# Optimization experiments

Hardware: AMD Instinct MI355X
Metric: run time of the kernel (lower is better)

Reference implementation:

```python
import jax, jax.numpy as jnp
import numpy as np

H = 1024      # hidden_dim
NH = 16       # num_heads
HD = H // NH  # head_dim
FF = 4 * H
EPS = 1e-5

def _ln(x, g, b):
    m = jnp.mean(x, axis=-1, keepdims=True)
    v = jnp.var(x, axis=-1, keepdims=True)
    return (x - m) * jax.lax.rsqrt(v + EPS) * g + b

def setup_inputs() -> dict:
    key = jax.random.key(0)
    ks = jax.random.split(key, 12)
    s = 1.0 / np.sqrt(H)
    inp = {
        'x': jax.random.normal(ks[0], (2, 2048, H), dtype=jnp.float32),
        'Wq': jax.random.normal(ks[1], (H, H), dtype=jnp.float32) * s,
        'bq': jnp.zeros((H,), dtype=jnp.float32),
        'Wk': jax.random.normal(ks[2], (H, H), dtype=jnp.float32) * s,
        'bk': jnp.zeros((H,), dtype=jnp.float32),
        'Wv': jax.random.normal(ks[3], (H, H), dtype=jnp.float32) * s,
        'bv': jnp.zeros((H,), dtype=jnp.float32),
        'Wo': jax.random.normal(ks[4], (H, H), dtype=jnp.float32) * s,
        'bo': jnp.zeros((H,), dtype=jnp.float32),
        'g1': jnp.ones((H,), dtype=jnp.float32),
        'b1': jnp.zeros((H,), dtype=jnp.float32),
        'W1': jax.random.normal(ks[5], (H, FF), dtype=jnp.float32) * s,
        'bf1': jnp.zeros((FF,), dtype=jnp.float32),
        'W2': jax.random.normal(ks[6], (FF, H), dtype=jnp.float32) * (1.0 / np.sqrt(FF)),
        'bf2': jnp.zeros((H,), dtype=jnp.float32),
        'g2': jnp.ones((H,), dtype=jnp.float32),
        'b2': jnp.zeros((H,), dtype=jnp.float32),
    }
    return inp

def reference(x, Wq, bq, Wk, bk, Wv, bv, Wo, bo, g1, b1, W1, bf1, W2, bf2, g2, b2):
    B, S, _ = x.shape
    residual = x
    xn = _ln(x, g1, b1)
    # [B,S,H] -> [B,NH,S,HD]
    def split_heads(t):
        return t.reshape(B, S, NH, HD).transpose(0, 2, 1, 3)
    q = split_heads(xn @ Wq + bq)
    k = split_heads(xn @ Wk + bk)
    v = split_heads(xn @ Wv + bv)
    scores = jnp.einsum('bhqd,bhkd->bhqk', q, k) / np.sqrt(HD).astype(np.float32)
    attn = jax.nn.softmax(scores, axis=-1)
    ctx = jnp.einsum('bhqk,bhkd->bhqd', attn, v)
    ctx = ctx.transpose(0, 2, 1, 3).reshape(B, S, H)
    out = ctx @ Wo + bo + residual
    residual = out
    on = _ln(out, g2, b2)
    out = jax.nn.relu(on @ W1 + bf1) @ W2 + bf2 + residual
    return out
```

## Files before the change

### kernel.cpp

```cpp
#include <hip/hip_runtime.h>
#include <hip/hip_bf16.h>

constexpr int HDIM = 1024;
constexpr int NHEAD = 16;
constexpr int FFDIM = 4096;
constexpr int SEQLEN = 2048;
constexpr int NTOK = 4096;

typedef __bf16 bf16x8 __attribute__((ext_vector_type(8)));
typedef float f32x4 __attribute__((ext_vector_type(4)));
typedef short s16x4 __attribute__((ext_vector_type(4)));

union U16x8 {
    s16x4 h[2];
    bf16x8 v;
    int4 raw;
    unsigned u[4];
    short s[8];
};

__device__ __forceinline__ short f2bf(float f) {
    union { float f; unsigned u; } c;
    c.f = f;
    return (short)((c.u + 0x8000u) >> 16);
}
__device__ __forceinline__ float bf2f(short s) {
    union { unsigned u; float f; } c;
    c.u = ((unsigned)(unsigned short)s) << 16;
    return c.f;
}

__device__ __forceinline__ unsigned cvtpk(float a, float b) {
    __hip_bfloat162 h = __float22bfloat162_rn(float2{a, b});
    return *reinterpret_cast<unsigned*>(&h);
}

__device__ __forceinline__ float exp2_raw(float x) {
    float r;
    asm("v_exp_f32 %0, %1" : "=v"(r) : "v"(x));
    return r;
}

template <int N>
__device__ __forceinline__ void wait_vmcnt() {
    if constexpr (N == 0) asm volatile("s_waitcnt vmcnt(0)" ::: "memory");
    else if constexpr (N == 8) asm volatile("s_waitcnt vmcnt(8)" ::: "memory");
    else if constexpr (N == 16) asm volatile("s_waitcnt vmcnt(16)" ::: "memory");
    else static_assert(N == 0 || N == 8 || N == 16, "unsupported vmcnt");
}
__device__ __forceinline__ void barrier_fence() {
    __builtin_amdgcn_s_barrier();
    asm volatile("" ::: "memory");
}

__device__ __forceinline__ void gload16(const void* gsrc, void* lds) {
    __builtin_amdgcn_global_load_lds(
        (const __attribute__((address_space(1))) unsigned int*)gsrc,
        (__attribute__((address_space(3))) unsigned int*)lds, 16, 0, 0);
}


constexpr float QSCALE = 0.18033688011112042f;

__device__ __forceinline__ void ln_store(float (&vv)[16], const float* g,
                                         const float* b, short* orow, int lane,
                                         float mean, float rstd) {
#pragma unroll
    for (int i = 0; i < 4; ++i) {
        const int c = i * 256 + lane * 4;
        float4 gv = *(const float4*)&g[c];
        float4 bv = *(const float4*)&b[c];
        union { s16x4 h4; uint2 u2; } pk;
        pk.u2.x = cvtpk((vv[i * 4 + 0] - mean) * rstd * gv.x + bv.x,
                        (vv[i * 4 + 1] - mean) * rstd * gv.y + bv.y);
        pk.u2.y = cvtpk((vv[i * 4 + 2] - mean) * rstd * gv.z + bv.z,
                        (vv[i * 4 + 3] - mean) * rstd * gv.w + bv.w);
        const int kk = c & 31;
        const int dst = (c & ~31) + ((kk & 15) >> 2) * 8 + (kk >> 4) * 4;
        *(s16x4*)&orow[dst] = pk.h4;
    }
}

__device__ __forceinline__ void ln_row(const float* __restrict__ xr,
                                       const float* __restrict__ g,
                                       const float* __restrict__ b,
                                       short* __restrict__ orow, int lane) {
    float vv[16];
    float s = 0.0f, ss = 0.0f;
#pragma unroll
    for (int i = 0; i < 4; ++i) {
        float4 v = *(const float4*)&xr[i * 256 + lane * 4];
        vv[i * 4] = v.x; vv[i * 4 + 1] = v.y; vv[i * 4 + 2] = v.z; vv[i * 4 + 3] = v.w;
        s += v.x + v.y + v.z + v.w;
        ss += v.x * v.x + v.y * v.y + v.z * v.z + v.w * v.w;
    }
#pragma unroll
    for (int o = 32; o > 0; o >>= 1) {
        s += __shfl_xor(s, o);
        ss += __shfl_xor(ss, o);
    }
    const float mean = s * (1.0f / HDIM);
    const float rstd = rsqrtf(ss * (1.0f / HDIM) - mean * mean + 1e-5f);
    ln_store(vv, g, b, orow, lane, mean, rstd);
}

__device__ __forceinline__ void ln_row_b(const short* __restrict__ xr,
                                         const float* __restrict__ g,
                                         const float* __restrict__ b,
                                         short* __restrict__ orow, int lane) {
    float vv[16];
    float s = 0.0f, ss = 0.0f;
#pragma unroll
    for (int i = 0; i < 4; ++i) {
        s16x4 h = *(const s16x4*)&xr[i * 256 + lane * 4];
#pragma unroll
        for (int j = 0; j < 4; ++j) {
            const float f = bf2f(h[j]);
            vv[i * 4 + j] = f;
            s += f;
            ss += f * f;
        }
    }
#pragma unroll
    for (int o = 32; o > 0; o >>= 1) {
        s += __shfl_xor(s, o);
        ss += __shfl_xor(ss, o);
    }
    const float mean = s * (1.0f / HDIM);
    const float rstd = rsqrtf(ss * (1.0f / HDIM) - mean * mean + 1e-5f);
    ln_store(vv, g, b, orow, lane, mean, rstd);
}

__global__ __launch_bounds__(256)
void wconv_all(const float* __restrict__ Wq, const float* __restrict__ Wk,
               const float* __restrict__ Wv, const float* __restrict__ Wo,
               const float* __restrict__ W1, const float* __restrict__ W2,
               short* __restrict__ qkvT, short* __restrict__ WoT,
               short* __restrict__ W1T, short* __restrict__ W2T,
               const float* __restrict__ x, const float* __restrict__ g1,
               const float* __restrict__ b1, short* __restrict__ xn) {
    int i = blockIdx.x;
    if (i >= 6144) {
        const int wave = threadIdx.x >> 6, lane = threadIdx.x & 63;
        const int row = (i - 6144) * 4 + wave;
        ln_row(x + (size_t)row * HDIM, g1, b1, xn + (size_t)row * HDIM, lane);
        return;
    }
    const float* W;
    short* WT;
    int K, N, bx, by;
    if (i < 2048) {
        const int w = i >> 9;
        i &= 511;
        K = HDIM; N = HDIM; bx = i & 3; by = i >> 2;
        W = w == 0 ? Wq : w == 1 ? Wk : w == 2 ? Wv : Wo;
        WT = w == 3 ? WoT : qkvT + (size_t)w * HDIM * HDIM;
    } else if (i < 4096) {
        i -= 2048;
        K = HDIM; N = FFDIM; bx = i & 15; by = i >> 4;
        W = W1; WT = W1T;
    } else {
        i -= 4096;
        K = FFDIM; N = HDIM; bx = i & 3; by = i >> 2;
        W = W2; WT = W2T;
    }
    const int n = bx * 256 + threadIdx.x;
    const int g = by >> 2, fc = by & 3;
    const int k0 = g * 32 + fc * 4;
    float a[4], c[4];
#pragma unroll
    for (int j = 0; j < 4; ++j) a[j] = W[(size_t)(k0 + j) * N + n];
#pragma unroll
    for (int j = 0; j < 4; ++j) c[j] = W[(size_t)(k0 + 16 + j) * N + n];
    U16x8 u;
    u.u[0] = cvtpk(a[0], a[1]);
    u.u[1] = cvtpk(a[2], a[3]);
    u.u[2] = cvtpk(c[0], c[1]);
    u.u[3] = cvtpk(c[2], c[3]);
    *(int4*)(WT + (size_t)n * K + by * 8) = u.raw;
}

__global__ __launch_bounds__(256)
void ln_bf16b(const short* __restrict__ x, const float* __restrict__ g,
              const float* __restrict__ b, short* __restrict__ out) {
    const int wave = threadIdx.x >> 6, lane = threadIdx.x & 63;
    const int row = blockIdx.x * 4 + wave;
    ln_row_b(x + (size_t)row * HDIM, g, b, out + (size_t)row * HDIM, lane);
}

template <int BM, int BN, int MODE, int PIPE>
__global__ __launch_bounds__(256, (PIPE == 3) ? 1 : (PIPE ? 2 : (((BM + BN) == 256) ? 3 : 4)))
void gemm_bf16(const short* __restrict__ A, const short* __restrict__ BT,
               const float* __restrict__ bias, const void* __restrict__ resid,
               void* __restrict__ outp, int M, int N, int K,
               const float* __restrict__ bias2, const float* __restrict__ bias3,
               void* __restrict__ out3) {
    constexpr int MI = BM / 32, NJ = BN / 32;
    constexpr int NSEG = (BM + BN) / 16;
    constexpr int PW = NSEG / 4;
    constexpr int BUFS = (BM + BN) * 32;
    constexpr int NBUF = (PIPE == 3) ? 8 : (PIPE == 2) ? 4 : 2;
    static_assert(PIPE < 2 || (BM + BN) == 256, "PIPE>=2 tuned for PW=4");
    __shared__ short LdsF[NBUF * BUFS];
    const int tid = threadIdx.x;
    const int lane = tid & 63, wave = tid >> 6;
    const int wm = wave >> 1, wn = wave & 1;
    const int l15 = lane & 15, lg = lane >> 4;
    const int lsw = lg ^ ((l15 >> 1) & 3);
    const int m0 = blockIdx.x * BM, n0 = blockIdx.y * BN;
    const int nk = K >> 5;
    const int sr = lane >> 2;
    const int sc8 = (((lane & 3) ^ ((sr >> 1) & 3))) * 8;

    auto stage = [&](int buf, int kt) {
#pragma unroll
        for (int p = 0; p < PW; ++p) {
            const int s = wave + p * 4;
            const short* src = (s < BM / 16)
                ? A + (size_t)(m0 + s * 16 + sr) * K + kt * 32 + sc8
                : BT + (size_t)(n0 + (s - BM / 16) * 16 + sr) * K + kt * 32 + sc8;
            const int off = __builtin_amdgcn_readfirstlane(buf * BUFS * 2 + s * 1024);
            gload16(src, (char*)LdsF + off);
        }
    };
    auto compute = [&](int buf, f32x4 (&acc)[MI][NJ]) {
        bf16x8 af[MI], bfr[NJ];
#pragma unroll
        for (int i = 0; i < MI; ++i)
            af[i] = *(const bf16x8*)&LdsF[buf * BUFS +
                                          (wm * (BM / 2) + i * 16 + l15) * 32 + lsw * 8];
#pragma unroll
        for (int j = 0; j < NJ; ++j)
            bfr[j] = *(const bf16x8*)&LdsF[buf * BUFS +
                                           (BM + wn * (BN / 2) + j * 16 + l15) * 32 + lsw * 8];
#pragma unroll
        for (int i = 0; i < MI; ++i)
#pragma unroll
            for (int j = 0; j < NJ; ++j)
                acc[i][j] = __builtin_amdgcn_mfma_f32_16x16x32_bf16(af[i], bfr[j], acc[i][j], 0, 0, 0);
    };

    f32x4 acc[MI][NJ] = {};
    if constexpr (PIPE == 0) {
        stage(0, 0);
        for (int kt = 0; kt < nk; ++kt) {
            const int buf = kt & 1;
            __syncthreads();
            if (kt + 1 < nk) stage(buf ^ 1, kt + 1);
            compute(buf, acc);
        }
    } else if constexpr (PIPE == 2) {
        stage(0, 0); stage(1, 1); stage(2, 2); stage(3, 3);
        const int np = nk >> 1;
        for (int t = 0; t < np; ++t) {
            const int pb = (t & 1) * 2;
            if (t + 1 < np) wait_vmcnt<8>();
            else wait_vmcnt<0>();
            barrier_fence();
            __builtin_amdgcn_s_setprio(1);
            compute(pb, acc);
            compute(pb + 1, acc);
            __builtin_amdgcn_s_setprio(0);
            if (t + 2 < np) {
                barrier_fence();
                stage(pb, 2 * t + 4);
                stage(pb + 1, 2 * t + 5);
            }
        }
    } else {
        stage(0, 0); stage(1, 1); stage(2, 2); stage(3, 3);
        stage(4, 4); stage(5, 5);
        const int np = nk >> 1;
        for (int t = 0; t < np; ++t) {
            const int pb = (t & 3) * 2;
            if (t + 2 < np) wait_vmcnt<16>();
            else if (t + 1 < np) wait_vmcnt<8>();
            else wait_vmcnt<0>();
            barrier_fence();
            if (t + 3 < np) {
                const int sb = ((t + 3) & 3) * 2;
                stage(sb, 2 * t + 6);
                stage(sb + 1, 2 * t + 7);
            }
            __builtin_amdgcn_s_setprio(1);
            compute(pb, acc);
            compute(pb + 1, acc);
            __builtin_amdgcn_s_setprio(0);
        }
    }

    const int rbase = m0 + wm * (BM / 2);
    const int cbase = n0 + wn * (BN / 2);
    if constexpr (MODE == 4) {
#pragma unroll
        for (int i = 0; i < MI; ++i)
#pragma unroll
            for (int j = 0; j < NJ; ++j) {
                const int c = cbase + j * 16 + l15;
                const float bv = bias[c];
#pragma unroll
                for (int ii = 0; ii < 4; ++ii) {
                    const int r = rbase + i * 16 + lg * 4 + ii;
                    const size_t idx = (size_t)r * N + c;
                    ((short*)outp)[idx] = f2bf(acc[i][j][ii] + bv + ((const float*)resid)[idx]);
                }
            }
    } else if constexpr (MODE == 5) {
#pragma unroll
        for (int i = 0; i < MI; ++i)
#pragma unroll
            for (int j = 0; j < NJ; ++j) {
                const int c = cbase + j * 16 + l15;
                const float bv = bias[c];
#pragma unroll
                for (int ii = 0; ii < 4; ++ii) {
                    const int r = rbase + i * 16 + lg * 4 + ii;
                    const size_t idx = (size_t)r * N + c;
                    ((float*)outp)[idx] = acc[i][j][ii] + bv + bf2f(((const short*)resid)[idx]);
                }
            }
    } else if constexpr (MODE == 1) {
#pragma unroll
        for (int i = 0; i < MI; ++i)
#pragma unroll
            for (int j = 0; j < NJ; ++j) {
                const int c = cbase + j * 16 + l15;
                const float bv = bias[c];
                const int cp = (c & ~31) | ((l15 >> 2) * 8 + (j & 1) * 4 + (l15 & 3));
#pragma unroll
                for (int ii = 0; ii < 4; ++ii) {
                    const int r = rbase + i * 16 + lg * 4 + ii;
                    float v = acc[i][j][ii] + bv;
                    v = v > 0.0f ? v : 0.0f;
                    ((short*)outp)[(size_t)r * N + cp] = f2bf(v);
                }
            }
    } else {
        const int which = n0 >> 10;
        if (which < 2) {
            const float* bb = which == 0 ? bias : bias2;
            const float qs = which == 0 ? QSCALE : 1.0f;
            short* QKp = (short*)outp;
#pragma unroll
            for (int i = 0; i < MI; ++i)
#pragma unroll
                for (int j = 0; j < NJ; ++j) {
                    const int c = cbase + j * 16 + l15;
                    const float bv = bb[c & 1023];
                    const int cp = (c & ~31) | ((l15 >> 2) * 8 + (j & 1) * 4 + (l15 & 3));
#pragma unroll
                    for (int ii = 0; ii < 4; ++ii) {
                        const int r = rbase + i * 16 + lg * 4 + ii;
                        QKp[(size_t)r * 2048 + cp] = f2bf((acc[i][j][ii] + bv) * qs);
                    }
                }
        } else {
            short* VTp = (short*)out3;
#pragma unroll
            for (int j = 0; j < NJ; ++j) {
                const int c = cbase + j * 16 + l15;
                const int cc = c - 2048;
                const int hh = cc >> 6, dd = cc & 63;
                const float bv = bias3[cc];
#pragma unroll
                for (int i = 0; i < MI; ++i) {
                    const int r0 = rbase + i * 16 + lg * 4;
                    const int bb_ = r0 >> 11;
                    const int s0 = r0 & (SEQLEN - 1);
                    const int sbase = (s0 & ~31) + lg * 8 + (i & 1) * 4;
                    union { s16x4 h4; uint2 u2; } pk;
                    pk.u2.x = cvtpk(acc[i][j][0] + bv, acc[i][j][1] + bv);
                    pk.u2.y = cvtpk(acc[i][j][2] + bv, acc[i][j][3] + bv);
                    *(s16x4*)&VTp[(((size_t)(bb_ * NHEAD + hh)) * 64 + dd) * SEQLEN + sbase] = pk.h4;
                }
            }
        }
    }
}

__global__ __launch_bounds__(256, 4)
void attn_fwd(const short* __restrict__ QK, const short* __restrict__ VT,
              short* __restrict__ ctx) {
    __shared__ short KlF[2 * 4096];
    __shared__ short VlF[2 * 4096];
    const int tid = threadIdx.x, lane = tid & 63, wave = tid >> 6;
    const int l15 = lane & 15, lg = lane >> 4;
    const int lsw = lg ^ ((l15 >> 1) & 3);
    const int bid = blockIdx.x;
    const int xcd = bid & 7, li = bid >> 3;
    const int bh = xcd * 4 + (li >> 5);
    const int qt = li & 31;
    const int b = bh >> 4, h = bh & 15;
    const size_t tokbase = (size_t)b * SEQLEN;
    const int sr = lane >> 2;
    const int sc8 = (((lane & 3) ^ ((sr >> 1) & 3))) * 8;

    const short* kp = QK + (tokbase + wave * 16 + sr) * 2048 + 1024 + h * 64 + sc8;
    const short* vp = VT + ((size_t)bh * 64 + wave * 16 + sr) * SEQLEN + sc8;

    auto stage = [&](int buf) {
        const int off = __builtin_amdgcn_readfirstlane(buf * 8192 + wave * 1024);
        gload16(kp, (char*)KlF + off);
        gload16(kp + 32, (char*)KlF + off + 4096);
        gload16(vp, (char*)VlF + off);
        gload16(vp + 32, (char*)VlF + off + 4096);
    };

    const short* qp = QK + (tokbase + qt * 64 + wave * 16 + l15) * 2048 + h * 64;
    bf16x8 qf[2];
    qf[0] = *(const bf16x8*)(qp + lg * 8);
    qf[1] = *(const bf16x8*)(qp + 32 + lg * 8);

    U16x8 uo;
#pragma unroll
    for (int j = 0; j < 8; ++j) uo.s[j] = 0x3F80;
    const bf16x8 onesv = uo.v;

    f32x4 o[4] = {};
    f32x4 Lacc = {};
    stage(0);
    for (int kt = 0; kt < SEQLEN / 64; ++kt) {
        const int buf = kt & 1;
        __syncthreads();
        if (kt + 1 < SEQLEN / 64) {
            kp += 64 * 2048;
            vp += 64;
            stage(buf ^ 1);
        }

        f32x4 sc[4];
        __builtin_amdgcn_s_setprio(1);
#pragma unroll
        for (int j = 0; j < 4; ++j) {
            bf16x8 kf0 = *(const bf16x8*)&KlF[buf * 4096 + (j * 16 + l15) * 32 + lsw * 8];
            bf16x8 kf1 = *(const bf16x8*)&KlF[buf * 4096 + 2048 + (j * 16 + l15) * 32 + lsw * 8];
            f32x4 z = {};
            z = __builtin_amdgcn_mfma_f32_16x16x32_bf16(kf0, qf[0], z, 0, 0, 0);
            sc[j] = __builtin_amdgcn_mfma_f32_16x16x32_bf16(kf1, qf[1], z, 0, 0, 0);
        }
        __builtin_amdgcn_s_setprio(0);

        U16x8 u0, u1;
        u0.u[0] = cvtpk(exp2_raw(sc[0][0]), exp2_raw(sc[0][1]));
        u0.u[1] = cvtpk(exp2_raw(sc[0][2]), exp2_raw(sc[0][3]));
        u0.u[2] = cvtpk(exp2_raw(sc[1][0]), exp2_raw(sc[1][1]));
        u0.u[3] = cvtpk(exp2_raw(sc[1][2]), exp2_raw(sc[1][3]));
        u1.u[0] = cvtpk(exp2_raw(sc[2][0]), exp2_raw(sc[2][1]));
        u1.u[1] = cvtpk(exp2_raw(sc[2][2]), exp2_raw(sc[2][3]));
        u1.u[2] = cvtpk(exp2_raw(sc[3][0]), exp2_raw(sc[3][1]));
        u1.u[3] = cvtpk(exp2_raw(sc[3][2]), exp2_raw(sc[3][3]));

        __builtin_amdgcn_s_setprio(1);
#pragma unroll
        for (int ks = 0; ks < 2; ++ks) {
            const bf16x8 pf = ks == 0 ? u0.v : u1.v;
            Lacc = __builtin_amdgcn_mfma_f32_16x16x32_bf16(onesv, pf, Lacc, 0, 0, 0);
#pragma unroll
            for (int fd = 0; fd < 4; ++fd) {
                bf16x8 vf = *(const bf16x8*)&VlF[buf * 4096 + ks * 2048 + (fd * 16 + l15) * 32 + lsw * 8];
                o[fd] = __builtin_amdgcn_mfma_f32_16x16x32_bf16(vf, pf, o[fd], 0, 0, 0);
            }
        }
        __builtin_amdgcn_s_setprio(0);
    }

    const float rl = 1.0f / Lacc[0];
    const int qrow = qt * 64 + wave * 16 + l15;
    short* crow = ctx + (tokbase + qrow) * HDIM + h * 64;
#pragma unroll
    for (int fd = 0; fd < 4; ++fd) {
        s16x4 v4;
#pragma unroll
        for (int ii = 0; ii < 4; ++ii) v4[ii] = f2bf(o[fd][ii] * rl);
        *(s16x4*)(crow + (fd >> 1) * 32 + lg * 8 + (fd & 1) * 4) = v4;
    }
}

extern "C" void kernel_launch(void* const* d_in, const int* in_sizes, int n_in,
                              void* d_out, int out_size, void* d_ws, size_t ws_size,
                              hipStream_t stream) {
    const float* x  = (const float*)d_in[0];
    const float* Wq = (const float*)d_in[1];
    const float* bq = (const float*)d_in[2];
    const float* Wk = (const float*)d_in[3];
    const float* bk = (const float*)d_in[4];
    const float* Wv = (const float*)d_in[5];
    const float* bv = (const float*)d_in[6];
    const float* Wo = (const float*)d_in[7];
    const float* bo = (const float*)d_in[8];
    const float* g1 = (const float*)d_in[9];
    const float* b1 = (const float*)d_in[10];
    const float* W1 = (const float*)d_in[11];
    const float* bf1 = (const float*)d_in[12];
    const float* W2 = (const float*)d_in[13];
    const float* bf2 = (const float*)d_in[14];
    const float* g2 = (const float*)d_in[15];
    const float* b2 = (const float*)d_in[16];

    char* ws = (char*)d_ws;
    const size_t MB = 1024 * 1024;
    short* qkvT = (short*)(ws + 0 * MB);
    short* WoT  = (short*)(ws + 6 * MB);
    short* W1T  = (short*)(ws + 8 * MB);
    short* W2T  = (short*)(ws + 16 * MB);
    short* xn   = (short*)(ws + 24 * MB);
    short* QKb  = (short*)(ws + 32 * MB);
    short* VTb  = (short*)(ws + 48 * MB);
    short* ctx  = (short*)(ws + 56 * MB);
    short* out1b = (short*)(ws + 64 * MB);
    short* h1   = (short*)(ws + 32 * MB);

    wconv_all<<<7168, 256, 0, stream>>>(Wq, Wk, Wv, Wo, W1, W2, qkvT, WoT, W1T,
                                        W2T, x, g1, b1, xn);

    gemm_bf16<128, 128, 2, 2><<<dim3(NTOK / 128, 3072 / 128), 256, 0, stream>>>(
        xn, qkvT, bq, nullptr, QKb, NTOK, 3072, HDIM, bk, bv, VTb);

    attn_fwd<<<1024, 256, 0, stream>>>(QKb, VTb, ctx);

    gemm_bf16<128, 128, 4, 3><<<dim3(NTOK / 128, HDIM / 128), 256, 0, stream>>>(
        ctx, WoT, bo, x, out1b, NTOK, HDIM, HDIM, nullptr, nullptr, nullptr);

    ln_bf16b<<<NTOK / 4, 256, 0, stream>>>(out1b, g2, b2, xn);

    gemm_bf16<128, 128, 1, 2><<<dim3(NTOK / 128, FFDIM / 128), 256, 0, stream>>>(
        xn, W1T, bf1, nullptr, h1, NTOK, FFDIM, HDIM, nullptr, nullptr, nullptr);

    gemm_bf16<128, 128, 5, 3><<<dim3(NTOK / 128, HDIM / 128), 256, 0, stream>>>(
        h1, W2T, bf2, out1b, (float*)d_out, NTOK, HDIM, FFDIM, nullptr, nullptr, nullptr);
}
```

Measured before the change: 211.7 us.

## Use 256x256 tile GEMM with 8 waves for the FFN up-projection

Adds a dedicated gemm256 kernel with 512 threads and 256x256 output tiles, each wave computing 128x64, for the W1 GEMM with fused bias+ReLU. Larger tiles raise arithmetic intensity and cut global/LDS traffic per MFMA. The trade-off is fewer blocks (256), lower occupancy and higher register use, and scalar bf16 stores in the epilogue. Unused PIPE==0 paths are also removed from the generic GEMM.

```diff
diff --git a/kernel.cpp b/kernel.cpp
--- a/kernel.cpp
+++ b/kernel.cpp
@@ -189,7 +189,7 @@
 }
 
 template <int BM, int BN, int MODE, int PIPE>
-__global__ __launch_bounds__(256, (PIPE == 3) ? 1 : (PIPE ? 2 : (((BM + BN) == 256) ? 3 : 4)))
+__global__ __launch_bounds__(256, (PIPE == 3) ? 1 : 2)
 void gemm_bf16(const short* __restrict__ A, const short* __restrict__ BT,
                const float* __restrict__ bias, const void* __restrict__ resid,
                void* __restrict__ outp, int M, int N, int K,
@@ -199,8 +199,7 @@
     constexpr int NSEG = (BM + BN) / 16;
     constexpr int PW = NSEG / 4;
     constexpr int BUFS = (BM + BN) * 32;
-    constexpr int NBUF = (PIPE == 3) ? 8 : (PIPE == 2) ? 4 : 2;
-    static_assert(PIPE < 2 || (BM + BN) == 256, "PIPE>=2 tuned for PW=4");
+    constexpr int NBUF = (PIPE == 3) ? 8 : 4;
     __shared__ short LdsF[NBUF * BUFS];
     const int tid = threadIdx.x;
     const int lane = tid & 63, wave = tid >> 6;
@@ -241,15 +240,7 @@
     };
 
     f32x4 acc[MI][NJ] = {};
-    if constexpr (PIPE == 0) {
-        stage(0, 0);
-        for (int kt = 0; kt < nk; ++kt) {
-            const int buf = kt & 1;
-            __syncthreads();
-            if (kt + 1 < nk) stage(buf ^ 1, kt + 1);
-            compute(buf, acc);
-        }
-    } else if constexpr (PIPE == 2) {
+    if constexpr (PIPE == 2) {
         stage(0, 0); stage(1, 1); stage(2, 2); stage(3, 3);
         const int np = nk >> 1;
         for (int t = 0; t < np; ++t) {
@@ -376,6 +367,91 @@
             }
         }
     }
+}
+
+__global__ __launch_bounds__(512, 1)
+void gemm256(const short* __restrict__ A, const short* __restrict__ BT,
+             const float* __restrict__ bias, short* __restrict__ outp,
+             int M, int N, int K) {
+    constexpr int BM = 256, BN = 256;
+    constexpr int MI = 8, NJ = 4;
+    constexpr int PW = 4;
+    constexpr int BUFS = (BM + BN) * 32;
+    __shared__ short LdsF[4 * BUFS];
+    const int tid = threadIdx.x;
+    const int lane = tid & 63, wave = tid >> 6;
+    const int wr = wave >> 2, wc = wave & 3;
+    const int l15 = lane & 15, lg = lane >> 4;
+    const int lsw = lg ^ ((l15 >> 1) & 3);
+    const int m0 = blockIdx.x * BM, n0 = blockIdx.y * BN;
+    const int nk = K >> 5;
+    const int sr = lane >> 2;
+    const int sc8 = (((lane & 3) ^ ((sr >> 1) & 3))) * 8;
+
+    auto stage = [&](int buf, int kt) {
+#pragma unroll
+        for (int p = 0; p < PW; ++p) {
+            const int s = wave + p * 8;
+            const short* src = (s < 16)
+                ? A + (size_t)(m0 + s * 16 + sr) * K + kt * 32 + sc8
+                : BT + (size_t)(n0 + (s - 16) * 16 + sr) * K + kt * 32 + sc8;
+            const int off = __builtin_amdgcn_readfirstlane(buf * BUFS * 2 + s * 1024);
+            gload16(src, (char*)LdsF + off);
+        }
+    };
+    auto compute = [&](int buf, f32x4 (&acc)[MI][NJ]) {
+        bf16x8 af[MI], bfr[NJ];
+#pragma unroll
+        for (int i = 0; i < MI; ++i)
+            af[i] = *(const bf16x8*)&LdsF[buf * BUFS +
+                                          (wr * 128 + i * 16 + l15) * 32 + lsw * 8];
+#pragma unroll
+        for (int j = 0; j < NJ; ++j)
+            bfr[j] = *(const bf16x8*)&LdsF[buf * BUFS +
+                                           (BM + wc * 64 + j * 16 + l15) * 32 + lsw * 8];
+#pragma unroll
+        for (int i = 0; i < MI; ++i)
+#pragma unroll
+            for (int j = 0; j < NJ; ++j)
+                acc[i][j] = __builtin_amdgcn_mfma_f32_16x16x32_bf16(af[i], bfr[j], acc[i][j], 0, 0, 0);
+    };
+
+    f32x4 acc[MI][NJ] = {};
+    stage(0, 0); stage(1, 1); stage(2, 2); stage(3, 3);
+    const int np = nk >> 1;
+    for (int t = 0; t < np; ++t) {
+        const int pb = (t & 1) * 2;
+        if (t + 1 < np) wait_vmcnt<8>();
+        else wait_vmcnt<0>();
+        barrier_fence();
+        __builtin_amdgcn_s_setprio(1);
+        compute(pb, acc);
+        compute(pb + 1, acc);
+        __builtin_amdgcn_s_setprio(0);
+        if (t + 2 < np) {
+            barrier_fence();
+            stage(pb, 2 * t + 4);
+            stage(pb + 1, 2 * t + 5);
+        }
+    }
+
+    const int rbase = m0 + wr * 128;
+    const int cbase = n0 + wc * 64;
+#pragma unroll
+    for (int i = 0; i < MI; ++i)
+#pragma unroll
+        for (int j = 0; j < NJ; ++j) {
+            const int c = cbase + j * 16 + l15;
+            const float bv = bias[c];
+            const int cp = (c & ~31) | ((l15 >> 2) * 8 + (j & 1) * 4 + (l15 & 3));
+#pragma unroll
+            for (int ii = 0; ii < 4; ++ii) {
+                const int r = rbase + i * 16 + lg * 4 + ii;
+                float v = acc[i][j][ii] + bv;
+                v = v > 0.0f ? v : 0.0f;
+                outp[(size_t)r * N + cp] = f2bf(v);
+            }
+        }
 }
 
 __global__ __launch_bounds__(256, 4)
@@ -523,8 +599,8 @@
 
     ln_bf16b<<<NTOK / 4, 256, 0, stream>>>(out1b, g2, b2, xn);
 
-    gemm_bf16<128, 128, 1, 2><<<dim3(NTOK / 128, FFDIM / 128), 256, 0, stream>>>(
-        xn, W1T, bf1, nullptr, h1, NTOK, FFDIM, HDIM, nullptr, nullptr, nullptr);
+    gemm256<<<dim3(NTOK / 256, FFDIM / 256), 512, 0, stream>>>(
+        xn, W1T, bf1, h1, NTOK, FFDIM, HDIM);
 
     gemm_bf16<128, 128, 5, 3><<<dim3(NTOK / 128, HDIM / 128), 256, 0, stream>>>(
         h1, W2T, bf2, out1b, (float*)d_out, NTOK, HDIM, FFDIM, nullptr, nullptr, nullptr);
```

After: 211.9 us (median of 2 runs). Within noise of the previous version (+0.1%).
